# Performance work log

Hardware: AMD Instinct MI355X
Metric: run time of the kernel (lower is better)

The kernel has to match this reference:

```python
import jax, jax.numpy as jnp
import numpy as np

N = 50000      # nodes
E = 600000     # edges
D_IN = 7       # input feature dim (Attn_head(7,128))
H = 128        # hidden dim
L = 2          # n_layer - 1 iterations actually executed


def _attn_head(x, edge_index, W, a1, a2, b, Wres):
    # GAT head over edge_index: h=xW; logit_e = leakyrelu(a1.h[src] + a2.h[dst]);
    # per-destination segment softmax; scatter-add aggregate; bias+residual+SELU.
    n = x.shape[0]
    h = x @ W                              # [N,H]
    src, dst = edge_index[0], edge_index[1]
    f1 = h @ a1                            # [N]
    f2 = h @ a2                            # [N]
    logits = jax.nn.leaky_relu(f1[src] + f2[dst], 0.2)   # [E]
    m = jax.ops.segment_max(logits, dst, num_segments=n)
    e = jnp.exp(logits - m[dst])
    s = jax.ops.segment_sum(e, dst, num_segments=n)
    coef = e / (s[dst] + 1e-9)             # [E] softmax over incoming edges
    out = jax.ops.segment_sum(coef[:, None] * h[src], dst, num_segments=n) + b
    res = x @ Wres if Wres is not None else x
    return jax.nn.selu(out + res)


def _simple_att(x3, Wa, ba, ua):
    # HAN-style attention pooling over axis 1. x3: [N,T,H]
    v = jnp.tanh(x3 @ Wa + ba)             # [N,T,H]
    vu = jnp.einsum('nth,h->nt', v, ua)    # [N,T]
    alphas = jax.nn.softmax(vu, axis=1)
    return jnp.einsum('nth,nt->nh', x3, alphas)  # [N,H]


def setup_inputs() -> dict:
    key = jax.random.key(0)
    ks = jax.random.split(key, 20)
    def rn(k, shape, s=0.1):
        return jax.random.normal(k, shape, dtype=jnp.float32) * s
    inp = {
        'x': jax.random.normal(ks[0], (N, D_IN), dtype=jnp.float32),
        'edge_index': jax.random.randint(ks[1], (2, E), 0, N, dtype=jnp.int64),
        # input GAT head (7 -> 128) with residual projection
        'W0': rn(ks[2], (D_IN, H)), 'a1_0': rn(ks[3], (H,)), 'a2_0': rn(ks[4], (H,)),
        'b0': jnp.zeros((H,), jnp.float32), 'Wr0': rn(ks[5], (D_IN, H)),
        # initial SimpleAttLayer
        'Wa0': rn(ks[6], (H, H)), 'ba0': jnp.zeros((H,), jnp.float32), 'ua0': rn(ks[7], (H,)),
        # L stacked final GAT heads (128 -> 128, identity residual)
        'Wf': rn(ks[8], (L, H, H)), 'a1f': rn(ks[9], (L, H)), 'a2f': rn(ks[10], (L, H)),
        'bf': jnp.zeros((L, H), jnp.float32),
        # L final SimpleAttLayers
        'Waf': rn(ks[11], (L, H, H)), 'baf': jnp.zeros((L, H), jnp.float32), 'uaf': rn(ks[12], (L, H)),
        # fc 128 -> 1
        'Wfc': rn(ks[13], (H, 1)), 'bfc': jnp.zeros((1,), jnp.float32),
    }
    return inp


def reference(x, edge_index, W0, a1_0, a2_0, b0, Wr0, Wa0, ba0, ua0,
              Wf, a1f, a2f, bf, Waf, baf, uaf, Wfc, bfc):
    h = _attn_head(x, edge_index, W0, a1_0, a2_0, b0, Wr0)       # [N,H]
    final = _simple_att(h[:, None, :], Wa0, ba0, ua0)            # [N,H]
    for i in range(L):
        lo = _attn_head(final, edge_index, Wf[i], a1f[i], a2f[i], bf[i], None)
        lo = _simple_att(lo[:, None, :], Waf[i], baf[i], uaf[i])
        final = final + lo
    y = final[-1] @ Wfc + bfc                                    # last node -> [1]
    return jax.nn.leaky_relu(y, 0.01)
```

## Files before the change

### kernel.cpp

```cpp
#include <hip/hip_runtime.h>

#define C0   8192
#define C1   2048
#define CE1  32768
#define CE2  2048
#define CBK  32
#define MB   1024

struct KP {
  const float* x; const int* ei;
  const float* W0; const float* a1_0; const float* a2_0; const float* b0; const float* Wr0;
  const float* Wf; const float* a1f; const float* a2f; const float* bf;
  const float* Wfc; const float* bfc;
  float* out;
  int N, E, t, nb1, nscan;
  int* cnt;
  float* wa;
  int* idx0; int* idx1; int* list0; int* list1;
  float* s0; float* acc0;
  int* e1s; int* e1d; int* e2s;
  int* cntblk; int* e2blk;
  float* f0; float* hh0; float* av10; float* av20;
  float* f1; float* hh1; float* av11; float* av21;
};

__device__ __forceinline__ float lrelu(float v, float a){ return v >= 0.f ? v : a*v; }
__device__ __forceinline__ float selu_f(float v){
  const float sc = 1.0507009873554805f, al = 1.6732632423543772f;
  return v > 0.f ? sc*v : sc*al*expm1f(v);
}
__device__ __forceinline__ void claim0(int* idx, int* list, int* cnt, int node,
                                       float* s, float* acc){
  if (atomicCAS(&idx[node], -1, -2) == -1){
    int slot = atomicAdd(cnt, 1);
    if (slot < C0){
      list[slot] = node;
      s[slot] = 0.f;
      float4* a = (float4*)(acc + (size_t)slot * 128);
      #pragma unroll
      for (int k = 0; k < 32; ++k) a[k] = make_float4(0.f,0.f,0.f,0.f);
      idx[node] = slot;
    }
  }
}
__device__ __forceinline__ void claim1(int* idx, int* list, int* cnt, int node){
  if (atomicCAS(&idx[node], -1, -2) == -1){
    int slot = atomicAdd(cnt, 1);
    if (slot < C1){ list[slot] = node; idx[node] = slot; }
  }
}

__global__ void k_init_scan1(KP p){
  int tid = threadIdx.x;
  if ((int)blockIdx.x < p.nb1){
    int u = blockIdx.x*256 + tid;
    if (u < p.N){ int v = (u == p.t) ? 0 : -1; p.idx0[u] = v; p.idx1[u] = v; }
    if (blockIdx.x == 0){
      if (tid < 7){
        float sA = 0.f, sB = 0.f;
        for (int k = 0; k < 128; ++k){ float wv = p.W0[tid*128+k]; sA += wv*p.a1_0[k]; sB += wv*p.a2_0[k]; }
        p.wa[tid] = sA; p.wa[8+tid] = sB;
      }
      if (tid < 128) p.acc0[tid] = 0.f;
      else if (tid == 128){
        p.s0[0] = 0.f; p.list0[0] = p.t; p.list1[0] = p.t;
        p.cnt[1] = 0; p.cnt[2] = 0; p.cnt[3] = 1; p.cnt[4] = 1; p.cnt[7] = 0;
      }
    }
    return;
  }
  __shared__ int lcnt;
  __shared__ int lbuf[CBK];
  int sb = blockIdx.x - p.nb1;
  if (tid == 0) lcnt = 0;
  __syncthreads();
  int gt = sb*256 + tid;
  int nv = p.E >> 2;
  const int4* d4 = (const int4*)(p.ei + p.E);
  if (gt < nv){
    int4 dv = d4[gt];
    #pragma unroll
    for (int m = 0; m < 4; ++m){
      if ((&dv.x)[m] == p.t){
        int pos = atomicAdd(&lcnt, 1);
        if (pos < CBK) lbuf[pos] = p.ei[4*gt + m];
      }
    }
  }
  if (sb == p.nscan-1 && tid < (p.E & 3)){
    int i = nv*4 + tid;
    if (p.ei[p.E + i] == p.t){
      int pos = atomicAdd(&lcnt, 1);
      if (pos < CBK) lbuf[pos] = p.ei[i];
    }
  }
  __syncthreads();
  int m = min(lcnt, CBK);
  if (tid == 0) p.cntblk[sb] = m;
  if (tid < m)  p.e2blk[sb*CBK + tid] = lbuf[tid];
}

__global__ void k_scan2(KP p){
  __shared__ int bm[2048];
  __shared__ int e2c;
  int tid = threadIdx.x;
  int bmw = (p.N + 31) >> 5;
  for (int i = tid; i < bmw; i += 256) bm[i] = 0;
  if (tid == 0) e2c = 0;
  __syncthreads();
  if (tid == 0) atomicOr(&bm[p.t>>5], 1 << (p.t & 31));
  for (int i = tid; i < p.nscan; i += 256){
    int c = min(p.cntblk[i], CBK);
    for (int j = 0; j < c; ++j){
      int s = p.e2blk[i*CBK + j];
      atomicOr(&bm[s>>5], 1 << (s & 31));
      if (blockIdx.x == 0){
        int slot = atomicAdd(&e2c, 1);
        if (slot < CE2) p.e2s[slot] = s;
        claim1(p.idx1, p.list1, &p.cnt[4], s);
        claim0(p.idx0, p.list0, &p.cnt[3], s, p.s0, p.acc0);
      }
    }
  }
  __syncthreads();
  if (blockIdx.x == 0 && tid == 0) p.cnt[2] = min(e2c, CE2);
  int gt = blockIdx.x*256 + tid;
  int nv = p.E >> 2;
  const int4* d4 = (const int4*)(p.ei + p.E);
  if (gt < nv){
    int4 dv = d4[gt];
    #pragma unroll
    for (int m = 0; m < 4; ++m){
      int dd = (&dv.x)[m];
      if ((bm[dd>>5] >> (dd & 31)) & 1){
        int s = p.ei[4*gt + m];
        int slot = atomicAdd(&p.cnt[1], 1);
        if (slot < CE1){ p.e1s[slot] = s; p.e1d[slot] = dd; }
        claim0(p.idx0, p.list0, &p.cnt[3], s, p.s0, p.acc0);
      }
    }
  }
  if (gt < (p.E & 3)){
    int i = nv*4 + gt;
    int dd = p.ei[p.E + i];
    if ((bm[dd>>5] >> (dd & 31)) & 1){
      int s = p.ei[i];
      int slot = atomicAdd(&p.cnt[1], 1);
      if (slot < CE1){ p.e1s[slot] = s; p.e1d[slot] = dd; }
      claim0(p.idx0, p.list0, &p.cnt[3], s, p.s0, p.acc0);
    }
  }
}

__global__ void k_scan3(KP p){
  __shared__ int bm[2048];
  int tid = threadIdx.x;
  int bmw = (p.N + 31) >> 5;
  for (int i = tid; i < bmw; i += 256) bm[i] = 0;
  __syncthreads();
  int n0 = min(p.cnt[3], C0);
  for (int i = tid; i < n0; i += 256){ int u = p.list0[i]; atomicOr(&bm[u>>5], 1 << (u & 31)); }
  __syncthreads();
  int gt = blockIdx.x*256 + tid;
  int lane = tid & 63;
  int nv = p.E >> 2;
  const int4* d4 = (const int4*)(p.ei + p.E);
  bool inb = gt < nv;
  int4 dv = make_int4(-1,-1,-1,-1);
  if (inb) dv = d4[gt];
  #pragma unroll
  for (int m = 0; m < 4; ++m){
    int dd = inb ? (&dv.x)[m] : -1;
    bool match = (dd >= 0) && ((bm[dd>>5] >> (dd & 31)) & 1);
    int sv = 0;
    if (match) sv = p.ei[4*gt + m];
    unsigned long long b = __ballot(match);
    while (b){
      int l = __ffsll((long long)b) - 1; b &= b - 1;
      int s = __shfl(sv, l), d = __shfl(dd, l);
      float f = 0.f;
      #pragma unroll
      for (int j = 0; j < 7; ++j) f += p.x[s*7+j]*p.wa[j] + p.x[d*7+j]*p.wa[8+j];
      float e = expf(lrelu(f, 0.2f));
      int id = p.idx0[d];
      if (id >= 0){
        float h0 = 0.f, h1 = 0.f;
        #pragma unroll
        for (int j = 0; j < 7; ++j){
          float xs = p.x[s*7+j];
          float2 w2 = *(const float2*)&p.W0[j*128 + 2*lane];
          h0 += xs*w2.x; h1 += xs*w2.y;
        }
        atomicAdd(&p.acc0[(size_t)id*128 + 2*lane    ], e*h0);
        atomicAdd(&p.acc0[(size_t)id*128 + 2*lane + 1], e*h1);
        if (lane == 0) atomicAdd(&p.s0[id], e);
      }
    }
  }
  if (gt < (p.E & 3)){
    int i = nv*4 + gt;
    int dd = p.ei[p.E + i];
    if ((bm[dd>>5] >> (dd & 31)) & 1){
      int s = p.ei[i];
      float f = 0.f;
      for (int j = 0; j < 7; ++j) f += p.x[s*7+j]*p.wa[j] + p.x[dd*7+j]*p.wa[8+j];
      float e = expf(lrelu(f, 0.2f));
      int id = p.idx0[dd];
      if (id >= 0){
        for (int k = 0; k < 128; ++k){
          float h = 0.f;
          for (int j = 0; j < 7; ++j) h += p.x[s*7+j]*p.W0[j*128+k];
          atomicAdd(&p.acc0[(size_t)id*128 + k], e*h);
        }
        atomicAdd(&p.s0[id], e);
      }
    }
  }
}

__global__ void __launch_bounds__(128) k_fin0(KP p){
  __shared__ float sf[128];
  __shared__ float2 red[128];
  int tid = threadIdx.x;
  int n0 = min(p.cnt[3], C0);
  for (int b = blockIdx.x; b < n0; b += gridDim.x){
    int u = p.list0[b];
    float res = 0.f;
    #pragma unroll
    for (int j = 0; j < 7; ++j) res += p.x[u*7+j]*p.Wr0[j*128+tid];
    float v = selu_f(p.acc0[(size_t)b*128+tid]/(p.s0[b]+1e-9f) + p.b0[tid] + res);
    p.f0[(size_t)b*128+tid] = v;
    sf[tid] = v;
    __syncthreads();
    float hv = 0.f;
    #pragma unroll 8
    for (int j = 0; j < 128; ++j) hv += sf[j]*p.Wf[j*128+tid];
    p.hh0[(size_t)b*128+tid] = hv;
    red[tid] = make_float2(hv*p.a1f[tid], hv*p.a2f[tid]);
    __syncthreads();
    for (int st = 64; st > 0; st >>= 1){
      if (tid < st){ red[tid].x += red[tid+st].x; red[tid].y += red[tid+st].y; }
      __syncthreads();
    }
    if (tid == 0){ p.av10[b] = red[0].x; p.av20[b] = red[0].y; }
    __syncthreads();
  }
}

__global__ void __launch_bounds__(128) k_fin1_l2(KP p){
  __shared__ float sf[128];
  __shared__ float2 rd2[128];
  __shared__ int   msrc[MB];
  __shared__ float mev[MB];
  __shared__ int   mcnt;
  int tid = threadIdx.x;
  int n1  = min(p.cnt[4], C1);
  int ne1 = min(p.cnt[1], CE1);
  for (int b = blockIdx.x; b < n1; b += gridDim.x){
    int u = p.list1[b];
    int i0u = p.idx0[u];
    if (tid == 0) mcnt = 0;
    __syncthreads();
    float av2u = (i0u >= 0) ? p.av20[i0u] : 0.f;
    for (int i = tid; i < ne1; i += 128){
      if (p.e1d[i] == u){
        int i0s = p.idx0[p.e1s[i]];
        if (i0s >= 0){
          float e = expf(lrelu(p.av10[i0s] + av2u, 0.2f));
          int pos = atomicAdd(&mcnt, 1);
          if (pos < MB){ msrc[pos] = i0s; mev[pos] = e; }
        }
      }
    }
    __syncthreads();
    int mc = min(mcnt, MB);
    float acc = 0.f, s1 = 0.f;
    for (int q = 0; q < mc; ++q){
      s1  += mev[q];
      acc += mev[q]*p.hh0[(size_t)msrc[q]*128 + tid];
    }
    float f0v = (i0u >= 0) ? p.f0[(size_t)i0u*128 + tid] : 0.f;
    float lo = selu_f(acc/(s1 + 1e-9f) + p.bf[tid] + f0v);
    float v = f0v + lo;
    p.f1[(size_t)b*128 + tid] = v;
    sf[tid] = v;
    __syncthreads();
    float hv = 0.f;
    #pragma unroll 8
    for (int j = 0; j < 128; ++j) hv += sf[j]*p.Wf[16384 + j*128 + tid];
    p.hh1[(size_t)b*128 + tid] = hv;
    rd2[tid] = make_float2(hv*p.a1f[128+tid], hv*p.a2f[128+tid]);
    __syncthreads();
    for (int st = 64; st > 0; st >>= 1){
      if (tid < st){ rd2[tid].x += rd2[tid+st].x; rd2[tid].y += rd2[tid+st].y; }
      __syncthreads();
    }
    if (tid == 0){ p.av11[b] = rd2[0].x; p.av21[b] = rd2[0].y; }
    __syncthreads();
  }
  __threadfence();
  __shared__ int lastf;
  if (tid == 0) lastf = (atomicAdd(&p.cnt[7], 1) == (int)gridDim.x - 1) ? 1 : 0;
  __syncthreads();
  if (!lastf) return;
  __threadfence();
  __shared__ float se[128];
  __shared__ int   si[128];
  __shared__ float redl[128];
  int ne2 = min(p.cnt[2], CE2);
  float av21t = p.av21[0];
  float acc = 0.f, s2 = 0.f;
  for (int base = 0; base < ne2; base += 128){
    int i = base + tid; float e = 0.f; int ii = -1;
    if (i < ne2){
      ii = p.idx1[p.e2s[i]];
      if (ii >= 0) e = expf(lrelu(p.av11[ii] + av21t, 0.2f));
    }
    se[tid] = e; si[tid] = ii;
    __syncthreads();
    int c = min(128, ne2 - base);
    for (int q = 0; q < c; ++q){
      if (si[q] >= 0){ s2 += se[q]; acc += se[q]*p.hh1[(size_t)si[q]*128 + tid]; }
    }
    __syncthreads();
  }
  float f1v = p.f1[tid];
  float lo = selu_f(acc/(s2+1e-9f) + p.bf[128+tid] + f1v);
  redl[tid] = (f1v + lo)*p.Wfc[tid];
  __syncthreads();
  for (int st = 64; st > 0; st >>= 1){
    if (tid < st) redl[tid] += redl[tid+st];
    __syncthreads();
  }
  if (tid == 0) p.out[0] = lrelu(redl[0] + p.bfc[0], 0.01f);
}

extern "C" void kernel_launch(void* const* d_in, const int* in_sizes, int n_in,
                              void* d_out, int out_size, void* d_ws, size_t ws_size,
                              hipStream_t stream){
  (void)n_in; (void)out_size;
  KP p;
  p.x    = (const float*)d_in[0];
  p.ei   = (const int*)  d_in[1];
  p.W0   = (const float*)d_in[2];
  p.a1_0 = (const float*)d_in[3];
  p.a2_0 = (const float*)d_in[4];
  p.b0   = (const float*)d_in[5];
  p.Wr0  = (const float*)d_in[6];
  p.Wf   = (const float*)d_in[10];
  p.a1f  = (const float*)d_in[11];
  p.a2f  = (const float*)d_in[12];
  p.bf   = (const float*)d_in[13];
  p.Wfc  = (const float*)d_in[17];
  p.bfc  = (const float*)d_in[18];
  p.out  = (float*)d_out;

  p.N = in_sizes[0] / 7;
  p.E = in_sizes[1] / 2;
  p.t = p.N - 1;
  p.nb1   = (p.N + 255) / 256;
  p.nscan = ((p.E >> 2) + 255) / 256;

  char* q = (char*)d_ws;
  auto alloc = [&](size_t bytes) -> void* {
    void* r = (void*)q;
    q += (bytes + 255) & ~(size_t)255;
    return r;
  };
  p.cnt   = (int*)  alloc(64);
  p.wa    = (float*)alloc(sizeof(float)*16);
  p.idx0  = (int*)  alloc(sizeof(int)*(size_t)p.N);
  p.idx1  = (int*)  alloc(sizeof(int)*(size_t)p.N);
  p.list0 = (int*)  alloc(sizeof(int)*C0);
  p.list1 = (int*)  alloc(sizeof(int)*C1);
  p.s0    = (float*)alloc(sizeof(float)*C0);
  p.acc0  = (float*)alloc(sizeof(float)*(size_t)C0*128);
  p.e1s   = (int*)  alloc(sizeof(int)*CE1);
  p.e1d   = (int*)  alloc(sizeof(int)*CE1);
  p.e2s   = (int*)  alloc(sizeof(int)*CE2);
  p.cntblk= (int*)  alloc(sizeof(int)*(size_t)p.nscan);
  p.e2blk = (int*)  alloc(sizeof(int)*(size_t)p.nscan*CBK);
  p.f0    = (float*)alloc(sizeof(float)*(size_t)C0*128);
  p.hh0   = (float*)alloc(sizeof(float)*(size_t)C0*128);
  p.av10  = (float*)alloc(sizeof(float)*C0);
  p.av20  = (float*)alloc(sizeof(float)*C0);
  p.f1    = (float*)alloc(sizeof(float)*(size_t)C1*128);
  p.hh1   = (float*)alloc(sizeof(float)*(size_t)C1*128);
  p.av11  = (float*)alloc(sizeof(float)*C1);
  p.av21  = (float*)alloc(sizeof(float)*C1);
  if ((size_t)(q - (char*)d_ws) > ws_size) return;

  k_init_scan1<<<p.nb1 + p.nscan, 256, 0, stream>>>(p);
  k_scan2     <<<p.nscan,         256, 0, stream>>>(p);
  k_scan3     <<<p.nscan,         256, 0, stream>>>(p);
  k_fin0      <<<192,             128, 0, stream>>>(p);
  k_fin1_l2   <<<32,              128, 0, stream>>>(p);
}
```

Before: 46.05 us.

## Fuse scan3 and finalize stages into one kernel with global atomic barriers

Merges the third edge scan, the layer-0 finalize and the layer-1 finalize into a single launch. Stages are separated by software grid barriers built from atomic counters, and blocks that are not needed for later stages exit early. Each 256-thread block now processes two nodes at a time, and the per-node edge buffer MB is halved to fit shared memory. This removes two kernel launch gaps, but the spin barrier requires all scan blocks to be resident at once (about 586 blocks) to avoid deadlock, and the smaller buffer lowers the cap on gathered edges per node.

```diff
diff --git a/kernel.cpp b/kernel.cpp
--- a/kernel.cpp
+++ b/kernel.cpp
@@ -5,7 +5,7 @@
 #define CE1  32768
 #define CE2  2048
 #define CBK  32
-#define MB   1024
+#define MB   512
 
 struct KP {
   const float* x; const int* ei;
@@ -13,7 +13,7 @@
   const float* Wf; const float* a1f; const float* a2f; const float* bf;
   const float* Wfc; const float* bfc;
   float* out;
-  int N, E, t, nb1, nscan;
+  int N, E, t, nb1, nscan, nw1, nw2;
   int* cnt;
   float* wa;
   int* idx0; int* idx1; int* list0; int* list1;
@@ -29,6 +29,20 @@
   const float sc = 1.0507009873554805f, al = 1.6732632423543772f;
   return v > 0.f ? sc*v : sc*al*expm1f(v);
 }
+__device__ __forceinline__ void bar_arrive(int* c){
+  __syncthreads();
+  __threadfence();
+  if (threadIdx.x == 0) atomicAdd(c, 1);
+}
+__device__ __forceinline__ void bar_wait(int* c, int target){
+  if (threadIdx.x == 0){
+    while (__hip_atomic_load(c, __ATOMIC_RELAXED, __HIP_MEMORY_SCOPE_AGENT) < target)
+      __builtin_amdgcn_s_sleep(8);
+  }
+  __syncthreads();
+  __threadfence();
+}
+
 __device__ __forceinline__ void claim0(int* idx, int* list, int* cnt, int node,
                                        float* s, float* acc){
   if (atomicCAS(&idx[node], -1, -2) == -1){
@@ -64,7 +78,8 @@
       if (tid < 128) p.acc0[tid] = 0.f;
       else if (tid == 128){
         p.s0[0] = 0.f; p.list0[0] = p.t; p.list1[0] = p.t;
-        p.cnt[1] = 0; p.cnt[2] = 0; p.cnt[3] = 1; p.cnt[4] = 1; p.cnt[7] = 0;
+        p.cnt[1] = 0; p.cnt[2] = 0; p.cnt[3] = 1; p.cnt[4] = 1;
+        p.cnt[7] = 0; p.cnt[8] = 0; p.cnt[9] = 0;
       }
     }
     return;
@@ -152,187 +167,212 @@
   }
 }
 
-__global__ void k_scan3(KP p){
+__global__ void __launch_bounds__(256) k_scan3_fin(KP p){
   __shared__ int bm[2048];
-  int tid = threadIdx.x;
-  int bmw = (p.N + 31) >> 5;
-  for (int i = tid; i < bmw; i += 256) bm[i] = 0;
-  __syncthreads();
-  int n0 = min(p.cnt[3], C0);
-  for (int i = tid; i < n0; i += 256){ int u = p.list0[i]; atomicOr(&bm[u>>5], 1 << (u & 31)); }
-  __syncthreads();
-  int gt = blockIdx.x*256 + tid;
-  int lane = tid & 63;
-  int nv = p.E >> 2;
-  const int4* d4 = (const int4*)(p.ei + p.E);
-  bool inb = gt < nv;
-  int4 dv = make_int4(-1,-1,-1,-1);
-  if (inb) dv = d4[gt];
-  #pragma unroll
-  for (int m = 0; m < 4; ++m){
-    int dd = inb ? (&dv.x)[m] : -1;
-    bool match = (dd >= 0) && ((bm[dd>>5] >> (dd & 31)) & 1);
-    int sv = 0;
-    if (match) sv = p.ei[4*gt + m];
-    unsigned long long b = __ballot(match);
-    while (b){
-      int l = __ffsll((long long)b) - 1; b &= b - 1;
-      int s = __shfl(sv, l), d = __shfl(dd, l);
-      float f = 0.f;
-      #pragma unroll
-      for (int j = 0; j < 7; ++j) f += p.x[s*7+j]*p.wa[j] + p.x[d*7+j]*p.wa[8+j];
-      float e = expf(lrelu(f, 0.2f));
-      int id = p.idx0[d];
-      if (id >= 0){
-        float h0 = 0.f, h1 = 0.f;
-        #pragma unroll
-        for (int j = 0; j < 7; ++j){
-          float xs = p.x[s*7+j];
-          float2 w2 = *(const float2*)&p.W0[j*128 + 2*lane];
-          h0 += xs*w2.x; h1 += xs*w2.y;
-        }
-        atomicAdd(&p.acc0[(size_t)id*128 + 2*lane    ], e*h0);
-        atomicAdd(&p.acc0[(size_t)id*128 + 2*lane + 1], e*h1);
-        if (lane == 0) atomicAdd(&p.s0[id], e);
-      }
-    }
-  }
-  if (gt < (p.E & 3)){
-    int i = nv*4 + gt;
-    int dd = p.ei[p.E + i];
-    if ((bm[dd>>5] >> (dd & 31)) & 1){
-      int s = p.ei[i];
-      float f = 0.f;
-      for (int j = 0; j < 7; ++j) f += p.x[s*7+j]*p.wa[j] + p.x[dd*7+j]*p.wa[8+j];
-      float e = expf(lrelu(f, 0.2f));
-      int id = p.idx0[dd];
-      if (id >= 0){
-        for (int k = 0; k < 128; ++k){
-          float h = 0.f;
-          for (int j = 0; j < 7; ++j) h += p.x[s*7+j]*p.W0[j*128+k];
-          atomicAdd(&p.acc0[(size_t)id*128 + k], e*h);
-        }
-        atomicAdd(&p.s0[id], e);
-      }
-    }
-  }
-}
-
-__global__ void __launch_bounds__(128) k_fin0(KP p){
-  __shared__ float sf[128];
-  __shared__ float2 red[128];
-  int tid = threadIdx.x;
-  int n0 = min(p.cnt[3], C0);
-  for (int b = blockIdx.x; b < n0; b += gridDim.x){
-    int u = p.list0[b];
-    float res = 0.f;
-    #pragma unroll
-    for (int j = 0; j < 7; ++j) res += p.x[u*7+j]*p.Wr0[j*128+tid];
-    float v = selu_f(p.acc0[(size_t)b*128+tid]/(p.s0[b]+1e-9f) + p.b0[tid] + res);
-    p.f0[(size_t)b*128+tid] = v;
-    sf[tid] = v;
-    __syncthreads();
-    float hv = 0.f;
-    #pragma unroll 8
-    for (int j = 0; j < 128; ++j) hv += sf[j]*p.Wf[j*128+tid];
-    p.hh0[(size_t)b*128+tid] = hv;
-    red[tid] = make_float2(hv*p.a1f[tid], hv*p.a2f[tid]);
-    __syncthreads();
-    for (int st = 64; st > 0; st >>= 1){
-      if (tid < st){ red[tid].x += red[tid+st].x; red[tid].y += red[tid+st].y; }
-      __syncthreads();
-    }
-    if (tid == 0){ p.av10[b] = red[0].x; p.av20[b] = red[0].y; }
-    __syncthreads();
-  }
-}
-
-__global__ void __launch_bounds__(128) k_fin1_l2(KP p){
-  __shared__ float sf[128];
-  __shared__ float2 rd2[128];
-  __shared__ int   msrc[MB];
-  __shared__ float mev[MB];
-  __shared__ int   mcnt;
-  int tid = threadIdx.x;
-  int n1  = min(p.cnt[4], C1);
-  int ne1 = min(p.cnt[1], CE1);
-  for (int b = blockIdx.x; b < n1; b += gridDim.x){
-    int u = p.list1[b];
-    int i0u = p.idx0[u];
-    if (tid == 0) mcnt = 0;
-    __syncthreads();
-    float av2u = (i0u >= 0) ? p.av20[i0u] : 0.f;
-    for (int i = tid; i < ne1; i += 128){
-      if (p.e1d[i] == u){
-        int i0s = p.idx0[p.e1s[i]];
-        if (i0s >= 0){
-          float e = expf(lrelu(p.av10[i0s] + av2u, 0.2f));
-          int pos = atomicAdd(&mcnt, 1);
-          if (pos < MB){ msrc[pos] = i0s; mev[pos] = e; }
-        }
-      }
-    }
-    __syncthreads();
-    int mc = min(mcnt, MB);
-    float acc = 0.f, s1 = 0.f;
-    for (int q = 0; q < mc; ++q){
-      s1  += mev[q];
-      acc += mev[q]*p.hh0[(size_t)msrc[q]*128 + tid];
-    }
-    float f0v = (i0u >= 0) ? p.f0[(size_t)i0u*128 + tid] : 0.f;
-    float lo = selu_f(acc/(s1 + 1e-9f) + p.bf[tid] + f0v);
-    float v = f0v + lo;
-    p.f1[(size_t)b*128 + tid] = v;
-    sf[tid] = v;
-    __syncthreads();
-    float hv = 0.f;
-    #pragma unroll 8
-    for (int j = 0; j < 128; ++j) hv += sf[j]*p.Wf[16384 + j*128 + tid];
-    p.hh1[(size_t)b*128 + tid] = hv;
-    rd2[tid] = make_float2(hv*p.a1f[128+tid], hv*p.a2f[128+tid]);
-    __syncthreads();
-    for (int st = 64; st > 0; st >>= 1){
-      if (tid < st){ rd2[tid].x += rd2[tid+st].x; rd2[tid].y += rd2[tid+st].y; }
-      __syncthreads();
-    }
-    if (tid == 0){ p.av11[b] = rd2[0].x; p.av21[b] = rd2[0].y; }
-    __syncthreads();
-  }
-  __threadfence();
-  __shared__ int lastf;
-  if (tid == 0) lastf = (atomicAdd(&p.cnt[7], 1) == (int)gridDim.x - 1) ? 1 : 0;
-  __syncthreads();
-  if (!lastf) return;
-  __threadfence();
+  __shared__ float  sf[2][128];
+  __shared__ float2 rd2[2][128];
+  __shared__ int   msrc[2][MB];
+  __shared__ float mev[2][MB];
+  __shared__ int   mcnt[2];
   __shared__ float se[128];
   __shared__ int   si[128];
   __shared__ float redl[128];
-  int ne2 = min(p.cnt[2], CE2);
-  float av21t = p.av21[0];
-  float acc = 0.f, s2 = 0.f;
-  for (int base = 0; base < ne2; base += 128){
-    int i = base + tid; float e = 0.f; int ii = -1;
-    if (i < ne2){
-      ii = p.idx1[p.e2s[i]];
-      if (ii >= 0) e = expf(lrelu(p.av11[ii] + av21t, 0.2f));
-    }
-    se[tid] = e; si[tid] = ii;
+  __shared__ int   lastf;
+  int tid = threadIdx.x;
+
+  {
+    int bmw = (p.N + 31) >> 5;
+    for (int i = tid; i < bmw; i += 256) bm[i] = 0;
     __syncthreads();
-    int c = min(128, ne2 - base);
-    for (int q = 0; q < c; ++q){
-      if (si[q] >= 0){ s2 += se[q]; acc += se[q]*p.hh1[(size_t)si[q]*128 + tid]; }
-    }
+    int n0 = min(p.cnt[3], C0);
+    for (int i = tid; i < n0; i += 256){ int u = p.list0[i]; atomicOr(&bm[u>>5], 1 << (u & 31)); }
     __syncthreads();
-  }
-  float f1v = p.f1[tid];
-  float lo = selu_f(acc/(s2+1e-9f) + p.bf[128+tid] + f1v);
-  redl[tid] = (f1v + lo)*p.Wfc[tid];
-  __syncthreads();
-  for (int st = 64; st > 0; st >>= 1){
-    if (tid < st) redl[tid] += redl[tid+st];
+    int gt = blockIdx.x*256 + tid;
+    int lane = tid & 63;
+    int nv = p.E >> 2;
+    const int4* d4 = (const int4*)(p.ei + p.E);
+    bool inb = gt < nv;
+    int4 dv = make_int4(-1,-1,-1,-1);
+    if (inb) dv = d4[gt];
+    #pragma unroll
+    for (int m = 0; m < 4; ++m){
+      int dd = inb ? (&dv.x)[m] : -1;
+      bool match = (dd >= 0) && ((bm[dd>>5] >> (dd & 31)) & 1);
+      int sv = 0;
+      if (match) sv = p.ei[4*gt + m];
+      unsigned long long b = __ballot(match);
+      while (b){
+        int l = __ffsll((long long)b) - 1; b &= b - 1;
+        int s = __shfl(sv, l), d = __shfl(dd, l);
+        float f = 0.f;
+        #pragma unroll
+        for (int j = 0; j < 7; ++j) f += p.x[s*7+j]*p.wa[j] + p.x[d*7+j]*p.wa[8+j];
+        float e = expf(lrelu(f, 0.2f));
+        int id = p.idx0[d];
+        if (id >= 0){
+          float h0 = 0.f, h1 = 0.f;
+          #pragma unroll
+          for (int j = 0; j < 7; ++j){
+            float xs = p.x[s*7+j];
+            float2 w2 = *(const float2*)&p.W0[j*128 + 2*lane];
+            h0 += xs*w2.x; h1 += xs*w2.y;
+          }
+          atomicAdd(&p.acc0[(size_t)id*128 + 2*lane    ], e*h0);
+          atomicAdd(&p.acc0[(size_t)id*128 + 2*lane + 1], e*h1);
+          if (lane == 0) atomicAdd(&p.s0[id], e);
+        }
+      }
+    }
+    if (gt < (p.E & 3)){
+      int i = nv*4 + gt;
+      int dd = p.ei[p.E + i];
+      if ((bm[dd>>5] >> (dd & 31)) & 1){
+        int s = p.ei[i];
+        float f = 0.f;
+        for (int j = 0; j < 7; ++j) f += p.x[s*7+j]*p.wa[j] + p.x[dd*7+j]*p.wa[8+j];
+        float e = expf(lrelu(f, 0.2f));
+        int id = p.idx0[dd];
+        if (id >= 0){
+          for (int k = 0; k < 128; ++k){
+            float h = 0.f;
+            for (int j = 0; j < 7; ++j) h += p.x[s*7+j]*p.W0[j*128+k];
+            atomicAdd(&p.acc0[(size_t)id*128 + k], e*h);
+          }
+          atomicAdd(&p.s0[id], e);
+        }
+      }
+    }
+  }
+  bar_arrive(&p.cnt[8]);
+  if ((int)blockIdx.x >= p.nw1) return;
+  bar_wait(&p.cnt[8], (int)gridDim.x);
+
+  {
+    int sub = tid >> 7, ch = tid & 127;
+    int n0 = min(p.cnt[3], C0);
+    for (int base = blockIdx.x*2; base < n0; base += p.nw1*2){
+      int b = base + sub; bool act = (b < n0);
+      float v = 0.f, hv = 0.f;
+      if (act){
+        int u = p.list0[b];
+        float res = 0.f;
+        #pragma unroll
+        for (int j = 0; j < 7; ++j) res += p.x[u*7+j]*p.Wr0[j*128+ch];
+        v = selu_f(p.acc0[(size_t)b*128+ch]/(p.s0[b]+1e-9f) + p.b0[ch] + res);
+        p.f0[(size_t)b*128+ch] = v;
+        sf[sub][ch] = v;
+      }
+      __syncthreads();
+      if (act){
+        #pragma unroll 8
+        for (int j = 0; j < 128; ++j) hv += sf[sub][j]*p.Wf[j*128+ch];
+        p.hh0[(size_t)b*128+ch] = hv;
+        rd2[sub][ch] = make_float2(hv*p.a1f[ch], hv*p.a2f[ch]);
+      } else rd2[sub][ch] = make_float2(0.f, 0.f);
+      __syncthreads();
+      for (int st = 64; st > 0; st >>= 1){
+        if (ch < st){ rd2[sub][ch].x += rd2[sub][ch+st].x; rd2[sub][ch].y += rd2[sub][ch+st].y; }
+        __syncthreads();
+      }
+      if (act && ch == 0){ p.av10[b] = rd2[sub][0].x; p.av20[b] = rd2[sub][0].y; }
+      __syncthreads();
+    }
+  }
+  bar_arrive(&p.cnt[9]);
+  if ((int)blockIdx.x >= p.nw2) return;
+  bar_wait(&p.cnt[9], p.nw1);
+
+  {
+    int sub = tid >> 7, ch = tid & 127;
+    int n1  = min(p.cnt[4], C1);
+    int ne1 = min(p.cnt[1], CE1);
+    for (int base = blockIdx.x*2; base < n1; base += p.nw2*2){
+      int b = base + sub; bool act = (b < n1);
+      int u = 0, i0u = -1;
+      if (act){ u = p.list1[b]; i0u = p.idx0[u]; }
+      if (ch == 0) mcnt[sub] = 0;
+      __syncthreads();
+      float av2u = (act && i0u >= 0) ? p.av20[i0u] : 0.f;
+      if (act){
+        for (int i = ch; i < ne1; i += 128){
+          if (p.e1d[i] == u){
+            int i0s = p.idx0[p.e1s[i]];
+            if (i0s >= 0){
+              float e = expf(lrelu(p.av10[i0s] + av2u, 0.2f));
+              int pos = atomicAdd(&mcnt[sub], 1);
+              if (pos < MB){ msrc[sub][pos] = i0s; mev[sub][pos] = e; }
+            }
+          }
+        }
+      }
+      __syncthreads();
+      float hv = 0.f;
+      if (act){
+        int mc = min(mcnt[sub], MB);
+        float acc = 0.f, s1 = 0.f;
+        for (int q = 0; q < mc; ++q){
+          s1  += mev[sub][q];
+          acc += mev[sub][q]*p.hh0[(size_t)msrc[sub][q]*128 + ch];
+        }
+        float f0v = (i0u >= 0) ? p.f0[(size_t)i0u*128 + ch] : 0.f;
+        float lo = selu_f(acc/(s1 + 1e-9f) + p.bf[ch] + f0v);
+        float v = f0v + lo;
+        p.f1[(size_t)b*128 + ch] = v;
+        sf[sub][ch] = v;
+      }
+      __syncthreads();
+      if (act){
+        #pragma unroll 8
+        for (int j = 0; j < 128; ++j) hv += sf[sub][j]*p.Wf[16384 + j*128 + ch];
+        p.hh1[(size_t)b*128 + ch] = hv;
+        rd2[sub][ch] = make_float2(hv*p.a1f[128+ch], hv*p.a2f[128+ch]);
+      } else rd2[sub][ch] = make_float2(0.f, 0.f);
+      __syncthreads();
+      for (int st = 64; st > 0; st >>= 1){
+        if (ch < st){ rd2[sub][ch].x += rd2[sub][ch+st].x; rd2[sub][ch].y += rd2[sub][ch+st].y; }
+        __syncthreads();
+      }
+      if (act && ch == 0){ p.av11[b] = rd2[sub][0].x; p.av21[b] = rd2[sub][0].y; }
+      __syncthreads();
+    }
+  }
+  __threadfence();
+  if (tid == 0) lastf = (atomicAdd(&p.cnt[7], 1) == p.nw2 - 1) ? 1 : 0;
+  __syncthreads();
+  if (!lastf) return;
+  __threadfence();
+  {
+    int ne2 = min(p.cnt[2], CE2);
+    float av21t = p.av21[0];
+    float acc = 0.f, s2 = 0.f;
+    for (int base = 0; base < ne2; base += 128){
+      int i = base + tid; float e = 0.f; int ii = -1;
+      if (tid < 128 && i < ne2){
+        ii = p.idx1[p.e2s[i]];
+        if (ii >= 0) e = expf(lrelu(p.av11[ii] + av21t, 0.2f));
+      }
+      if (tid < 128){ se[tid] = e; si[tid] = ii; }
+      __syncthreads();
+      int c = min(128, ne2 - base);
+      if (tid < 128){
+        for (int q = 0; q < c; ++q){
+          if (si[q] >= 0){ s2 += se[q]; acc += se[q]*p.hh1[(size_t)si[q]*128 + tid]; }
+        }
+      }
+      __syncthreads();
+    }
+    if (tid < 128){
+      float f1v = p.f1[tid];
+      float lo = selu_f(acc/(s2+1e-9f) + p.bf[128+tid] + f1v);
+      redl[tid] = (f1v + lo)*p.Wfc[tid];
+    }
     __syncthreads();
-  }
-  if (tid == 0) p.out[0] = lrelu(redl[0] + p.bfc[0], 0.01f);
+    for (int st = 64; st > 0; st >>= 1){
+      if (tid < st) redl[tid] += redl[tid+st];
+      __syncthreads();
+    }
+    if (tid == 0) p.out[0] = lrelu(redl[0] + p.bfc[0], 0.01f);
+  }
 }
 
 extern "C" void kernel_launch(void* const* d_in, const int* in_sizes, int n_in,
@@ -360,6 +400,8 @@
   p.t = p.N - 1;
   p.nb1   = (p.N + 255) / 256;
   p.nscan = ((p.E >> 2) + 255) / 256;
+  p.nw1   = p.nscan < 192 ? p.nscan : 192;
+  p.nw2   = p.nw1 < 16 ? p.nw1 : 16;
 
   char* q = (char*)d_ws;
   auto alloc = [&](size_t bytes) -> void* {
@@ -392,7 +434,5 @@
 
   k_init_scan1<<<p.nb1 + p.nscan, 256, 0, stream>>>(p);
   k_scan2     <<<p.nscan,         256, 0, stream>>>(p);
-  k_scan3     <<<p.nscan,         256, 0, stream>>>(p);
-  k_fin0      <<<192,             128, 0, stream>>>(p);
-  k_fin1_l2   <<<32,              128, 0, stream>>>(p);
-}
+  k_scan3_fin <<<p.nscan,         256, 0, stream>>>(p);
+}
```

Measured after the change: 124.5 us. 170% more time.
